# Kernel optimization log

Hardware: AMD Instinct MI355X
Metric: run time of the kernel (lower is better)

The kernel has to match this reference:

```python
import jax, jax.numpy as jnp
import numpy as np

B, IN, OUT, K = 2048, 1024, 1024, 20


def setup_inputs() -> dict:
    key = jax.random.key(0)
    k1, k2 = jax.random.split(key)
    x = jax.random.normal(k1, (B, IN), dtype=jnp.float32)
    # per-output, per-input spline coefficients: (out_features, in_features, num_knots)
    W = jax.random.normal(k2, (OUT, IN, K), dtype=jnp.float32) * 0.1
    # evenly spaced knot grid on [-2, 2] (linspace)
    knots = jnp.linspace(-2.0, 2.0, K, dtype=jnp.float32)
    return {"x": x, "W": W, "knots": knots}


def reference(x, W, knots):
    # RBF spline basis shared across all output features (this is the fusion
    # the original per-output Python loop misses):
    # basis[b, i, k] = exp(-0.5 * ((x[b, i] - knots[k]) / h)^2)
    h = knots[1] - knots[0]  # uniform knot spacing -> RBF bandwidth
    basis = jnp.exp(-0.5 * jnp.square((x[:, :, None] - knots) / h))  # (B, IN, K)
    # Each SplineLayer o computes sum_{i,k} W[o,i,k] * basis[b,i,k]; the
    # KANBlock concatenates the OUT scalars -> a single einsum.
    return jnp.einsum("bik,oik->bo", basis, W)  # (B, OUT)
```

## Files before the change

### kernel.cpp

```cpp
#include <hip/hip_runtime.h>

#define B_DIM 2048
#define IN_DIM 1024
#define OUT_DIM 1024
#define K_KNOTS 20
#define KR (IN_DIM * K_KNOTS)
#define OUT_ELEMS (B_DIM * OUT_DIM)

#define TM 128
#define TN 128
#define BK 128
#define KSPLIT 4
#define MT_TILES (B_DIM / TM)
#define NT_TILES (OUT_DIM / TN)
#define GEMM_BLOCKS (MT_TILES * NT_TILES * KSPLIT)
#define LDS_AS0 0
#define LDS_AS1 8192
#define LDS_BS0 16384
#define LDS_BS1 24576

#define NB_QUADS (B_DIM * IN_DIM * 5)
#define NB_BASIS_BLK (NB_QUADS / 256)
#define NW4 (OUT_DIM * KR / 8)
#define NB_W_BLK (NW4 / 256)

typedef __bf16 bf16x8 __attribute__((ext_vector_type(8)));
typedef float  f32x4  __attribute__((ext_vector_type(4)));

#define MFMA16(a, b, c) __builtin_amdgcn_mfma_f32_16x16x32_bf16(a, b, c, 0, 0, 0)

__device__ __forceinline__ unsigned short f2bf(float f) {
    unsigned int u = __float_as_uint(f);
    unsigned int r = u + 0x7fffu + ((u >> 16) & 1u);
    return (unsigned short)(r >> 16);
}

__device__ __forceinline__ unsigned int pack2(float lo, float hi) {
    return (unsigned int)f2bf(lo) | ((unsigned int)f2bf(hi) << 16);
}

__device__ __forceinline__ void async_load16(const void* g, void* l) {
    __builtin_amdgcn_global_load_lds(
        (const __attribute__((address_space(1))) void*)g,
        (__attribute__((address_space(3))) void*)l,
        16, 0, 0);
}

__global__ void zero_out_kernel(float* out) {
    int idx = (blockIdx.x * 256 + threadIdx.x) * 4;
    float4 z = {0.f, 0.f, 0.f, 0.f};
    *(float4*)(out + idx) = z;
}

__global__ void __launch_bounds__(256) prep_kernel(
        const float* __restrict__ x,
        const float4* __restrict__ Wsrc,
        const float* __restrict__ knots,
        uint2* __restrict__ basis_out,
        uint4* __restrict__ w_out) {
    if (blockIdx.x < NB_BASIS_BLK) {
        unsigned int n = blockIdx.x * 256 + threadIdx.x;
        unsigned int q  = n % 5u;
        unsigned int bi = n / 5u;
        float t0 = knots[0];
        float h  = knots[1] - t0;
        float invh = 1.0f / h;
        float xv = x[bi];
        float k0 = (float)(4 * q);
        float v[4];
#pragma unroll
        for (int j = 0; j < 4; ++j) {
            float t = __builtin_fmaf(k0 + (float)j, h, t0);
            float d = (xv - t) * invh;
            v[j] = __expf(-0.5f * d * d);
        }
        uint2 o;
        o.x = pack2(v[0], v[1]);
        o.y = pack2(v[2], v[3]);
        basis_out[n] = o;
    } else {
        unsigned int t = (blockIdx.x - NB_BASIS_BLK) * 256 + threadIdx.x;
        float4 a = Wsrc[2 * t];
        float4 b = Wsrc[2 * t + 1];
        uint4 o;
        o.x = pack2(a.x, a.y);
        o.y = pack2(a.z, a.w);
        o.z = pack2(b.x, b.y);
        o.w = pack2(b.z, b.w);
        w_out[t] = o;
    }
}

#define AOFF(s, h) (((s) * 2 + (h)) * 8192)
#define BOFF(s, h) (32768 + ((s) * 2 + (h)) * 8192)

template <int S>
__device__ __forceinline__ void tile_step(
        int t, int ntiles,
        const unsigned short* __restrict__ Ab,
        const unsigned short* __restrict__ Bb,
        unsigned short* lds,
        f32x4 (&acc)[8][4],
        int m0, int n0, int k0,
        int wave, int wm, int wn, int r15, int c0, int c1,
        int srow8, int scol) {
    const int aB  = S * 16384 + (wm * 128 + r15) * 64;
    const int bB  = 32768 + S * 16384 + (wn * 64 + r15) * 64;
    const int kb1 = k0 + (t + 1) * 64;
    const int kb2 = k0 + (t + 2) * 64;

    auto stage = [&](const unsigned short* __restrict__ src, int grow, int kb, int lbase) {
        const unsigned short* g = src + (size_t)(grow + wave * 16 + srow8) * KR + kb + scol;
        async_load16(g,                  &lds[lbase + wave * 1024]);
        async_load16(g + (size_t)8 * KR, &lds[lbase + wave * 1024 + 512]);
    };

    if (t + 1 < ntiles) {
        stage(Bb, n0 + 128, kb1, BOFF(S ^ 1, 1));
        stage(Ab, m0 + 128, kb1, AOFF(S ^ 1, 1));
    }

    bf16x8 aR[4][2], bR[4][2], aS[4][2];
#pragma unroll
    for (int i = 0; i < 4; ++i) {
        aR[i][0] = *(const bf16x8*)&lds[aB + i * 1024 + c0];
        aR[i][1] = *(const bf16x8*)&lds[aB + i * 1024 + c1];
    }
#pragma unroll
    for (int j = 0; j < 2; ++j) {
        bR[j][0] = *(const bf16x8*)&lds[bB + j * 1024 + c0];
        bR[j][1] = *(const bf16x8*)&lds[bB + j * 1024 + c1];
    }
#pragma unroll
    for (int j = 2; j < 4; ++j) {
        bR[j][0] = *(const bf16x8*)&lds[bB + j * 1024 + c0];
        bR[j][1] = *(const bf16x8*)&lds[bB + j * 1024 + c1];
    }
#pragma unroll
    for (int i = 0; i < 2; ++i) {
        aS[i][0] = *(const bf16x8*)&lds[aB + (4 + i) * 1024 + c0];
        aS[i][1] = *(const bf16x8*)&lds[aB + (4 + i) * 1024 + c1];
    }

    asm volatile("s_waitcnt lgkmcnt(8)" ::: "memory");
    __builtin_amdgcn_sched_barrier(0);
    __builtin_amdgcn_s_setprio(1);
#pragma unroll
    for (int i = 0; i < 4; ++i)
#pragma unroll
        for (int j = 0; j < 2; ++j) {
            acc[i][j] = MFMA16(aR[i][0], bR[j][0], acc[i][j]);
            acc[i][j] = MFMA16(aR[i][1], bR[j][1], acc[i][j]);
        }
    __builtin_amdgcn_s_setprio(0);

#pragma unroll
    for (int i = 2; i < 4; ++i) {
        aS[i][0] = *(const bf16x8*)&lds[aB + (4 + i) * 1024 + c0];
        aS[i][1] = *(const bf16x8*)&lds[aB + (4 + i) * 1024 + c1];
    }

    asm volatile("s_waitcnt lgkmcnt(4)" ::: "memory");
    __builtin_amdgcn_sched_barrier(0);
    __builtin_amdgcn_s_setprio(1);
#pragma unroll
    for (int i = 0; i < 4; ++i)
#pragma unroll
        for (int j = 2; j < 4; ++j) {
            acc[i][j] = MFMA16(aR[i][0], bR[j][0], acc[i][j]);
            acc[i][j] = MFMA16(aR[i][1], bR[j][1], acc[i][j]);
        }
    __builtin_amdgcn_s_setprio(0);

    asm volatile("s_waitcnt lgkmcnt(0)" ::: "memory");
    __builtin_amdgcn_sched_barrier(0);
    __builtin_amdgcn_s_barrier();
    __builtin_amdgcn_sched_barrier(0);

    if (t + 2 < ntiles) {
        stage(Bb, n0, kb2, BOFF(S, 0));
        stage(Ab, m0, kb2, AOFF(S, 0));
    }

    __builtin_amdgcn_s_setprio(1);
#pragma unroll
    for (int i = 0; i < 4; ++i)
#pragma unroll
        for (int j = 2; j < 4; ++j) {
            acc[4 + i][j] = MFMA16(aS[i][0], bR[j][0], acc[4 + i][j]);
            acc[4 + i][j] = MFMA16(aS[i][1], bR[j][1], acc[4 + i][j]);
        }
#pragma unroll
    for (int i = 0; i < 4; ++i)
#pragma unroll
        for (int j = 0; j < 2; ++j) {
            acc[4 + i][j] = MFMA16(aS[i][0], bR[j][0], acc[4 + i][j]);
            acc[4 + i][j] = MFMA16(aS[i][1], bR[j][1], acc[4 + i][j]);
        }
    __builtin_amdgcn_s_setprio(0);

    if (t < ntiles - 2) asm volatile("s_waitcnt vmcnt(4)" ::: "memory");
    else                asm volatile("s_waitcnt vmcnt(0)" ::: "memory");
    __builtin_amdgcn_s_barrier();
}

template <int KS, bool ATOMIC>
__global__ void __launch_bounds__(512, 2)
kan_gemm8(const unsigned short* __restrict__ Ab,
          const unsigned short* __restrict__ Bb,
          float* __restrict__ out) {
    __shared__ __align__(16) unsigned short lds[65536];

    constexpr int KPBk   = KR / KS;
    constexpr int NTILES = KPBk / 64;

    const int id  = blockIdx.x;
    const int z   = id & 7;
    const int ord = id >> 3;
    const int mt  = ord & 7;
    const int nt  = ord >> 3;
    const int m0  = mt * 256;
    const int n0  = nt * 256;
    const int k0  = z * KPBk;

    const int tid  = threadIdx.x;
    const int wave = tid >> 6;
    const int lane = tid & 63;
    const int wm   = wave >> 2;
    const int wn   = wave & 3;

    const int srow8 = lane >> 3;
    const int scol  = ((lane & 7) ^ srow8) * 8;

    auto stage = [&](const unsigned short* __restrict__ src, int grow, int kb, int lbase) {
        const unsigned short* g = src + (size_t)(grow + wave * 16 + srow8) * KR + kb + scol;
        async_load16(g,                  &lds[lbase + wave * 1024]);
        async_load16(g + (size_t)8 * KR, &lds[lbase + wave * 1024 + 512]);
    };

    f32x4 acc[8][4];
#pragma unroll
    for (int i = 0; i < 8; ++i)
#pragma unroll
        for (int j = 0; j < 4; ++j) acc[i][j] = (f32x4){0.f, 0.f, 0.f, 0.f};

    const int q   = lane >> 4;
    const int r15 = lane & 15;
    const int r7  = lane & 7;
    const int c0  = (q ^ r7) * 8;
    const int c1  = ((4 + q) ^ r7) * 8;

    stage(Ab, m0,       k0,      AOFF(0, 0));
    stage(Ab, m0 + 128, k0,      AOFF(0, 1));
    stage(Bb, n0,       k0,      BOFF(0, 0));
    stage(Bb, n0 + 128, k0,      BOFF(0, 1));
    stage(Bb, n0,       k0 + 64, BOFF(1, 0));
    stage(Ab, m0,       k0 + 64, AOFF(1, 0));
    asm volatile("s_waitcnt vmcnt(4)" ::: "memory");
    __builtin_amdgcn_s_barrier();

    for (int tt = 0; tt < NTILES; tt += 2) {
        tile_step<0>(tt,     NTILES, Ab, Bb, lds, acc, m0, n0, k0,
                     wave, wm, wn, r15, c0, c1, srow8, scol);
        tile_step<1>(tt + 1, NTILES, Ab, Bb, lds, acc, m0, n0, k0,
                     wave, wm, wn, r15, c0, c1, srow8, scol);
    }

    float* dst = ATOMIC ? out : out + (size_t)z * OUT_ELEMS;
#pragma unroll
    for (int i = 0; i < 8; ++i)
#pragma unroll
        for (int j = 0; j < 4; ++j)
#pragma unroll
            for (int r = 0; r < 4; ++r) {
                const int row = m0 + wm * 128 + i * 16 + q * 4 + r;
                const int c   = n0 + wn * 64  + j * 16 + r15;
                if (ATOMIC)
                    atomicAdd(&dst[(size_t)row * OUT_DIM + c], acc[i][j][r]);
                else
                    dst[(size_t)row * OUT_DIM + c] = acc[i][j][r];
            }
}

template <int KS, bool ATOMIC>
__global__ void __launch_bounds__(256)
kan_gemm(const unsigned short* __restrict__ Ab,
         const unsigned short* __restrict__ Bb,
         float* __restrict__ out) {
    __shared__ __align__(16) unsigned short lds[32768];

    const int KPBk = KR / KS;
    const int id   = blockIdx.x;
    const int xcd  = id & 7;
    const int ord  = id >> 3;
    const int mt   = xcd * 2 + (ord & 1);
    const int nt   = (ord >> 1) & (NT_TILES - 1);
    const int z    = ord >> 4;
    const int m0 = mt * TM;
    const int n0 = nt * TN;
    const int k0 = z * KPBk;

    const int tid  = threadIdx.x;
    const int wave = tid >> 6;
    const int lane = tid & 63;
    const int wm = wave & 1;
    const int wn = wave >> 1;

    const int srow = lane >> 3;
    const int scol = ((lane & 7) ^ srow) * 8;

    f32x4 acc[4][4];
#pragma unroll
    for (int i = 0; i < 4; ++i)
#pragma unroll
        for (int j = 0; j < 4; ++j) acc[i][j] = (f32x4){0.f, 0.f, 0.f, 0.f};

    for (int kt = 0; kt < KPBk; kt += BK) {
        const int kb = k0 + kt;
        __syncthreads();
#pragma unroll
        for (int c = 0; c < 4; ++c) {
            const int chunk = wave * 4 + c;
            const int r = chunk * 8 + srow;
            const unsigned short* arow = Ab + (size_t)(m0 + r) * KR + kb + scol;
            const unsigned short* brow = Bb + (size_t)(n0 + r) * KR + kb + scol;
            unsigned short* slot = &lds[chunk * 512];
            async_load16(arow,      slot + LDS_AS0);
            async_load16(arow + 64, slot + LDS_AS1);
            async_load16(brow,      slot + LDS_BS0);
            async_load16(brow + 64, slot + LDS_BS1);
        }
        __syncthreads();

        const int quad = lane >> 4;
        const int r15  = lane & 15;
        const int r7   = lane & 7;
#pragma unroll
        for (int s = 0; s < 4; ++s) {
            const int abase = (s >> 1) ? LDS_AS1 : LDS_AS0;
            const int bbase = (s >> 1) ? LDS_BS1 : LDS_BS0;
            const int cg = (s & 1) * 4 + quad;
            const int xo = (cg ^ r7) * 8;
            bf16x8 af[4], bfv[4];
#pragma unroll
            for (int i = 0; i < 4; ++i) {
                af[i]  = *(const bf16x8*)&lds[abase + (wm * 64 + i * 16 + r15) * 64 + xo];
                bfv[i] = *(const bf16x8*)&lds[bbase + (wn * 64 + i * 16 + r15) * 64 + xo];
            }
#pragma unroll
            for (int i = 0; i < 4; ++i)
#pragma unroll
                for (int j = 0; j < 4; ++j)
                    acc[i][j] = MFMA16(af[i], bfv[j], acc[i][j]);
        }
    }

    float* dst = ATOMIC ? out : out + (size_t)z * OUT_ELEMS;
    const int quad = lane >> 4;
    const int col  = lane & 15;
#pragma unroll
    for (int i = 0; i < 4; ++i)
#pragma unroll
        for (int j = 0; j < 4; ++j)
#pragma unroll
            for (int r = 0; r < 4; ++r) {
                const int row = m0 + wm * 64 + i * 16 + quad * 4 + r;
                const int c   = n0 + wn * 64 + j * 16 + col;
                if (ATOMIC)
                    atomicAdd(&dst[(size_t)row * OUT_DIM + c], acc[i][j][r]);
                else
                    dst[(size_t)row * OUT_DIM + c] = acc[i][j][r];
            }
}

template <int KS>
__global__ void kan_reduce(const float* __restrict__ part, float* __restrict__ out) {
    const int idx = (blockIdx.x * 256 + threadIdx.x) * 4;
    f32x4 s = *(const f32x4*)(part + idx);
#pragma unroll
    for (int z = 1; z < KS; ++z)
        s += *(const f32x4*)(part + (size_t)z * OUT_ELEMS + idx);
    *(f32x4*)(out + idx) = s;
}

__global__ void kan_fallback(const float* __restrict__ x,
                             const float* __restrict__ W,
                             const float* __restrict__ knots,
                             float* __restrict__ out) {
    __shared__ float basis[256 * K_KNOTS];
    const int b = blockIdx.x;
    const int o = blockIdx.y * blockDim.x + threadIdx.x;
    const float invh = 1.0f / (knots[1] - knots[0]);
    const float* w = W + (size_t)o * KR;
    float sum = 0.f;
    for (int i0 = 0; i0 < IN_DIM; i0 += 256) {
        __syncthreads();
        for (int idx = threadIdx.x; idx < 256 * K_KNOTS; idx += blockDim.x) {
            const int i = i0 + idx / K_KNOTS;
            const int k = idx % K_KNOTS;
            const float d = (x[(size_t)b * IN_DIM + i] - knots[k]) * invh;
            basis[idx] = __expf(-0.5f * d * d);
        }
        __syncthreads();
        for (int r = 0; r < 256 * K_KNOTS; ++r)
            sum += basis[r] * w[(size_t)i0 * K_KNOTS + r];
    }
    out[(size_t)b * OUT_DIM + o] = sum;
}

extern "C" void kernel_launch(void* const* d_in, const int* in_sizes, int n_in,
                              void* d_out, int out_size, void* d_ws, size_t ws_size,
                              hipStream_t stream) {
    const float* x     = (const float*)d_in[0];
    const float* W     = (const float*)d_in[1];
    const float* knots = (const float*)d_in[2];
    float* out = (float*)d_out;

    const size_t basis_bytes = (size_t)B_DIM * KR * 2;
    const size_t wb_bytes    = (size_t)OUT_DIM * KR * 2;
    const size_t part8_bytes = (size_t)8 * OUT_ELEMS * 4;
    const size_t part4_bytes = (size_t)4 * OUT_ELEMS * 4;

    unsigned short* Ab = (unsigned short*)d_ws;
    unsigned short* Bb = (unsigned short*)((char*)d_ws + basis_bytes);
    float* part = (float*)((char*)d_ws + basis_bytes + wb_bytes);

    if (ws_size >= basis_bytes + wb_bytes + part8_bytes) {
        prep_kernel<<<dim3(NB_BASIS_BLK + NB_W_BLK), dim3(256), 0, stream>>>(
            x, (const float4*)W, knots, (uint2*)Ab, (uint4*)Bb);
        kan_gemm8<8, false><<<dim3(256), dim3(512), 0, stream>>>(Ab, Bb, part);
        kan_reduce<8><<<dim3(OUT_ELEMS / (256 * 4)), dim3(256), 0, stream>>>(part, out);
    } else if (ws_size >= basis_bytes + wb_bytes + part4_bytes) {
        prep_kernel<<<dim3(NB_BASIS_BLK + NB_W_BLK), dim3(256), 0, stream>>>(
            x, (const float4*)W, knots, (uint2*)Ab, (uint4*)Bb);
        kan_gemm<4, false><<<dim3(GEMM_BLOCKS), dim3(256), 0, stream>>>(Ab, Bb, part);
        kan_reduce<4><<<dim3(OUT_ELEMS / (256 * 4)), dim3(256), 0, stream>>>(part, out);
    } else if (ws_size >= basis_bytes + wb_bytes) {
        zero_out_kernel<<<dim3(OUT_ELEMS / (256 * 4)), dim3(256), 0, stream>>>(out);
        prep_kernel<<<dim3(NB_BASIS_BLK + NB_W_BLK), dim3(256), 0, stream>>>(
            x, (const float4*)W, knots, (uint2*)Ab, (uint4*)Bb);
        kan_gemm8<8, true><<<dim3(256), dim3(512), 0, stream>>>(Ab, Bb, out);
    } else {
        kan_fallback<<<dim3(B_DIM, OUT_DIM / 256), dim3(256), 0, stream>>>(x, W, knots, out);
    }
}
```

Baseline: 257.3 us.

## Restructure GEMM tile step into four barrier-separated phases with simpler prefetch

```diff
diff --git a/kernel.cpp b/kernel.cpp
--- a/kernel.cpp
+++ b/kernel.cpp
@@ -107,7 +107,7 @@
     const int aB  = S * 16384 + (wm * 128 + r15) * 64;
     const int bB  = 32768 + S * 16384 + (wn * 64 + r15) * 64;
     const int kb1 = k0 + (t + 1) * 64;
-    const int kb2 = k0 + (t + 2) * 64;
+    const bool st = (t + 1 < ntiles);
 
     auto stage = [&](const unsigned short* __restrict__ src, int grow, int kb, int lbase) {
         const unsigned short* g = src + (size_t)(grow + wave * 16 + srow8) * KR + kb + scol;
@@ -115,92 +115,73 @@
         async_load16(g + (size_t)8 * KR, &lds[lbase + wave * 1024 + 512]);
     };
 
-    if (t + 1 < ntiles) {
-        stage(Bb, n0 + 128, kb1, BOFF(S ^ 1, 1));
-        stage(Ab, m0 + 128, kb1, AOFF(S ^ 1, 1));
-    }
-
-    bf16x8 aR[4][2], bR[4][2], aS[4][2];
-#pragma unroll
-    for (int i = 0; i < 4; ++i) {
-        aR[i][0] = *(const bf16x8*)&lds[aB + i * 1024 + c0];
-        aR[i][1] = *(const bf16x8*)&lds[aB + i * 1024 + c1];
-    }
-#pragma unroll
-    for (int j = 0; j < 2; ++j) {
-        bR[j][0] = *(const bf16x8*)&lds[bB + j * 1024 + c0];
-        bR[j][1] = *(const bf16x8*)&lds[bB + j * 1024 + c1];
-    }
-#pragma unroll
-    for (int j = 2; j < 4; ++j) {
-        bR[j][0] = *(const bf16x8*)&lds[bB + j * 1024 + c0];
-        bR[j][1] = *(const bf16x8*)&lds[bB + j * 1024 + c1];
-    }
-#pragma unroll
-    for (int i = 0; i < 2; ++i) {
-        aS[i][0] = *(const bf16x8*)&lds[aB + (4 + i) * 1024 + c0];
-        aS[i][1] = *(const bf16x8*)&lds[aB + (4 + i) * 1024 + c1];
-    }
-
-    asm volatile("s_waitcnt lgkmcnt(8)" ::: "memory");
+    bf16x8 a0[4], a1[4], b0[4], b1[4], s0[4], s1[4];
+
+#pragma unroll
+    for (int i = 0; i < 4; ++i) a0[i] = *(const bf16x8*)&lds[aB + i * 1024 + c0];
+#pragma unroll
+    for (int j = 0; j < 4; ++j) b0[j] = *(const bf16x8*)&lds[bB + j * 1024 + c0];
+    __builtin_amdgcn_s_barrier();
+    asm volatile("s_waitcnt lgkmcnt(0)" ::: "memory");
     __builtin_amdgcn_sched_barrier(0);
     __builtin_amdgcn_s_setprio(1);
 #pragma unroll
     for (int i = 0; i < 4; ++i)
 #pragma unroll
-        for (int j = 0; j < 2; ++j) {
-            acc[i][j] = MFMA16(aR[i][0], bR[j][0], acc[i][j]);
-            acc[i][j] = MFMA16(aR[i][1], bR[j][1], acc[i][j]);
-        }
+        for (int j = 0; j < 4; ++j)
+            acc[i][j] = MFMA16(a0[i], b0[j], acc[i][j]);
     __builtin_amdgcn_s_setprio(0);
 
 #pragma unroll
-    for (int i = 2; i < 4; ++i) {
-        aS[i][0] = *(const bf16x8*)&lds[aB + (4 + i) * 1024 + c0];
-        aS[i][1] = *(const bf16x8*)&lds[aB + (4 + i) * 1024 + c1];
-    }
-
-    asm volatile("s_waitcnt lgkmcnt(4)" ::: "memory");
+    for (int i = 0; i < 4; ++i) a1[i] = *(const bf16x8*)&lds[aB + i * 1024 + c1];
+#pragma unroll
+    for (int j = 0; j < 4; ++j) b1[j] = *(const bf16x8*)&lds[bB + j * 1024 + c1];
+    __builtin_amdgcn_s_barrier();
+    asm volatile("s_waitcnt lgkmcnt(0)" ::: "memory");
     __builtin_amdgcn_sched_barrier(0);
     __builtin_amdgcn_s_setprio(1);
 #pragma unroll
     for (int i = 0; i < 4; ++i)
 #pragma unroll
-        for (int j = 2; j < 4; ++j) {
-            acc[i][j] = MFMA16(aR[i][0], bR[j][0], acc[i][j]);
-            acc[i][j] = MFMA16(aR[i][1], bR[j][1], acc[i][j]);
-        }
+        for (int j = 0; j < 4; ++j)
+            acc[i][j] = MFMA16(a1[i], b1[j], acc[i][j]);
     __builtin_amdgcn_s_setprio(0);
 
+#pragma unroll
+    for (int i = 0; i < 4; ++i) s0[i] = *(const bf16x8*)&lds[aB + (4 + i) * 1024 + c0];
+    if (st) {
+        stage(Ab, m0,       kb1, AOFF(S ^ 1, 0));
+        stage(Ab, m0 + 128, kb1, AOFF(S ^ 1, 1));
+    }
+    __builtin_amdgcn_s_barrier();
     asm volatile("s_waitcnt lgkmcnt(0)" ::: "memory");
     __builtin_amdgcn_sched_barrier(0);
-    __builtin_amdgcn_s_barrier();
+    __builtin_amdgcn_s_setprio(1);
+#pragma unroll
+    for (int i = 0; i < 4; ++i)
+#pragma unroll
+        for (int j = 0; j < 4; ++j)
+            acc[4 + i][j] = MFMA16(s0[i], b0[j], acc[4 + i][j]);
+    __builtin_amdgcn_s_setprio(0);
+
+#pragma unroll
+    for (int i = 0; i < 4; ++i) s1[i] = *(const bf16x8*)&lds[aB + (4 + i) * 1024 + c1];
+    if (st) {
+        stage(Bb, n0,       kb1, BOFF(S ^ 1, 0));
+        stage(Bb, n0 + 128, kb1, BOFF(S ^ 1, 1));
+    }
+    __builtin_amdgcn_s_barrier();
+    asm volatile("s_waitcnt lgkmcnt(0)" ::: "memory");
     __builtin_amdgcn_sched_barrier(0);
-
-    if (t + 2 < ntiles) {
-        stage(Bb, n0, kb2, BOFF(S, 0));
-        stage(Ab, m0, kb2, AOFF(S, 0));
-    }
-
     __builtin_amdgcn_s_setprio(1);
 #pragma unroll
     for (int i = 0; i < 4; ++i)
 #pragma unroll
-        for (int j = 2; j < 4; ++j) {
-            acc[4 + i][j] = MFMA16(aS[i][0], bR[j][0], acc[4 + i][j]);
-            acc[4 + i][j] = MFMA16(aS[i][1], bR[j][1], acc[4 + i][j]);
-        }
-#pragma unroll
-    for (int i = 0; i < 4; ++i)
-#pragma unroll
-        for (int j = 0; j < 2; ++j) {
-            acc[4 + i][j] = MFMA16(aS[i][0], bR[j][0], acc[4 + i][j]);
-            acc[4 + i][j] = MFMA16(aS[i][1], bR[j][1], acc[4 + i][j]);
-        }
+        for (int j = 0; j < 4; ++j)
+            acc[4 + i][j] = MFMA16(s1[i], b1[j], acc[4 + i][j]);
     __builtin_amdgcn_s_setprio(0);
 
-    if (t < ntiles - 2) asm volatile("s_waitcnt vmcnt(4)" ::: "memory");
-    else                asm volatile("s_waitcnt vmcnt(0)" ::: "memory");
+    if (st) asm volatile("s_waitcnt vmcnt(0)" ::: "memory");
     __builtin_amdgcn_s_barrier();
 }
 
@@ -250,13 +231,11 @@
     const int c0  = (q ^ r7) * 8;
     const int c1  = ((4 + q) ^ r7) * 8;
 
-    stage(Ab, m0,       k0,      AOFF(0, 0));
-    stage(Ab, m0 + 128, k0,      AOFF(0, 1));
-    stage(Bb, n0,       k0,      BOFF(0, 0));
-    stage(Bb, n0 + 128, k0,      BOFF(0, 1));
-    stage(Bb, n0,       k0 + 64, BOFF(1, 0));
-    stage(Ab, m0,       k0 + 64, AOFF(1, 0));
-    asm volatile("s_waitcnt vmcnt(4)" ::: "memory");
+    stage(Ab, m0,       k0, AOFF(0, 0));
+    stage(Ab, m0 + 128, k0, AOFF(0, 1));
+    stage(Bb, n0,       k0, BOFF(0, 0));
+    stage(Bb, n0 + 128, k0, BOFF(0, 1));
+    asm volatile("s_waitcnt vmcnt(0)" ::: "memory");
     __builtin_amdgcn_s_barrier();
 
     for (int tt = 0; tt < NTILES; tt += 2) {
```

Result: no change. 257.3 us (+0.0%).
